# Optimization experiments

Measured on AMD Instinct MI355X. Metric: run time of the kernel, lower is better.

The kernel has to match this reference:

```python
import jax, jax.numpy as jnp
import numpy as np

N, E, G = 50000, 800000, 512
HD, ED, GD, HID = 128, 64, 64, 128  # h_dim, e_dim, g_dim, hid_dim


def _mlp2(x, W1, b1, W2, b2, last_act):
    # Linear -> ReLU -> Linear (-> optional last activation)
    y = jax.nn.relu(x @ W1 + b1) @ W2 + b2
    return last_act(y) if last_act is not None else y


def setup_inputs() -> dict:
    key = jax.random.key(0)
    ks = list(jax.random.split(key, 24))
    ki = iter(ks)

    def p(shape):
        return (jax.random.normal(next(ki), shape, jnp.float32) * 0.02)

    inp = {
        "h": jax.random.normal(next(ki), (N, HD), jnp.float32),
        "e_index": jax.random.randint(next(ki), (2, E), 0, N),
        "e": jax.random.normal(next(ki), (E, ED), jnp.float32),
        "g": jax.random.normal(next(ki), (G, GD), jnp.float32),
        "batch": jnp.sort(jax.random.randint(next(ki), (N,), 0, G)),
        # fc_m: [2*HD+ED+GD, HID, HID], last_activation=relu
        "W_m1": p((2 * HD + ED + GD, HID)), "b_m1": jnp.zeros((HID,), jnp.float32),
        "W_m2": p((HID, HID)), "b_m2": jnp.zeros((HID,), jnp.float32),
        # fc_m_att: [HID, 1], sigmoid
        "W_ma": p((HID, 1)), "b_ma": jnp.zeros((1,), jnp.float32),
        # fc_e: [HID, ED, ED]
        "W_e1": p((HID, ED)), "b_e1": jnp.zeros((ED,), jnp.float32),
        "W_e2": p((ED, ED)), "b_e2": jnp.zeros((ED,), jnp.float32),
        # fc_h: [HD+HID+GD, HD, HD]
        "W_h1": p((HD + HID + GD, HD)), "b_h1": jnp.zeros((HD,), jnp.float32),
        "W_h2": p((HD, HD)), "b_h2": jnp.zeros((HD,), jnp.float32),
        # fc_h_att: [HD, 1]
        "W_ha": p((HD, 1)), "b_ha": jnp.zeros((1,), jnp.float32),
        # fc_g: [GD+HD, GD, GD]
        "W_g1": p((GD + HD, GD)), "b_g1": jnp.zeros((GD,), jnp.float32),
        "W_g2": p((GD, GD)), "b_g2": jnp.zeros((GD,), jnp.float32),
    }
    return inp


def reference(h, e_index, e, g, batch,
              W_m1, b_m1, W_m2, b_m2, W_ma, b_ma,
              W_e1, b_e1, W_e2, b_e2,
              W_h1, b_h1, W_h2, b_h2, W_ha, b_ha,
              W_g1, b_g1, W_g2, b_g2):
    src, dst = e_index[0], e_index[1]
    e_batch = batch[dst]

    # edge message: concat gathered endpoints + edge feat + gathered global
    m_cat = jnp.concatenate([h[src], h[dst], e, g[e_batch]], axis=1)  # [E, 2HD+ED+GD]
    m = jax.nn.relu(jax.nn.relu(m_cat @ W_m1 + b_m1) @ W_m2 + b_m2)   # [E, HID]
    m_att = jax.nn.sigmoid(m @ W_ma + b_ma)                            # [E, 1]

    e_update = _mlp2(m, W_e1, b_e1, W_e2, b_e2, None)                  # [E, ED]
    e_out = jax.nn.relu(e + e_update)

    m_aggr = jax.ops.segment_sum(m_att * m, dst, num_segments=h.shape[0])  # [N, HID]

    h_cat = jnp.concatenate([h, m_aggr, g[batch]], axis=1)             # [N, HD+HID+GD]
    h_update = _mlp2(h_cat, W_h1, b_h1, W_h2, b_h2, None)
    h_out = jax.nn.relu(h + h_update)                                  # [N, HD]
    h_att = h_out @ W_ha + b_ha                                        # [N, 1]

    h_aggr = jax.ops.segment_sum(h_att * h_out, batch, num_segments=g.shape[0])  # [G, HD]

    g_cat = jnp.concatenate([g, h_aggr], axis=1)                       # [G, GD+HD]
    g_update = _mlp2(g_cat, W_g1, b_g1, W_g2, b_g2, None)
    g_out = jax.nn.relu(g + g_update)

    return (h_out, e_out, g_out)
```

## Files before the change

### kernel.cpp

```cpp
#include <hip/hip_runtime.h>
#include <hip/hip_bf16.h>

#define NN 50000
#define NE 800000
#define NG 512
#define HD 128
#define ED 64
#define GD 64
#define HID 128

typedef __attribute__((ext_vector_type(8))) short short8;
typedef __attribute__((ext_vector_type(4))) float f32x4;

__device__ __forceinline__ short f2bf(float f) {
  union { float f; unsigned u; } v; v.f = f;
  unsigned r = v.u + 0x7fffu + ((v.u >> 16) & 1u);
  return (short)(r >> 16);
}

__device__ __forceinline__ float bf2f(short s) {
  union { unsigned u; float f; } v;
  v.u = ((unsigned)(unsigned short)s) << 16;
  return v.f;
}

__device__ __forceinline__ short8 load_a8(const float* p) {
  const f32x4* q = (const f32x4*)p;
  f32x4 x0 = q[0], x1 = q[1];
  short8 r;
  r[0]=f2bf(x0[0]); r[1]=f2bf(x0[1]); r[2]=f2bf(x0[2]); r[3]=f2bf(x0[3]);
  r[4]=f2bf(x1[0]); r[5]=f2bf(x1[1]); r[6]=f2bf(x1[2]); r[7]=f2bf(x1[3]);
  return r;
}

__device__ __forceinline__ int swz(int row, int col, int rowBytes) {
  int b = row * rowBytes + col * 2;
  b ^= (row & 7) << 4;
  return b >> 1;
}

__global__ void pack_kernel(const float* __restrict__ Wm1, const float* __restrict__ Wm2,
                            const float* __restrict__ We1, const float* __restrict__ We2,
                            const float* __restrict__ Wh1, const float* __restrict__ Wh2,
                            short* __restrict__ out) {
  int gid = blockIdx.x * 256 + threadIdx.x;
  if (gid >= 135168) return;
  const float* W; int Ncol, base, idx;
  if (gid < 49152)       { W = Wm1; Ncol = 128; base = 0;      idx = gid; }
  else if (gid < 65536)  { W = Wm2; Ncol = 128; base = 49152;  idx = gid - 49152; }
  else if (gid < 73728)  { W = We1; Ncol = 64;  base = 65536;  idx = gid - 65536; }
  else if (gid < 77824)  { W = We2; Ncol = 64;  base = 73728;  idx = gid - 73728; }
  else if (gid < 118784) { W = Wh1; Ncol = 128; base = 77824;  idx = gid - 77824; }
  else                   { W = Wh2; Ncol = 128; base = 118784; idx = gid - 118784; }
  int k = idx / Ncol, n = idx % Ncol;
  out[base + (k >> 3) * Ncol * 8 + n * 8 + (k & 7)] = f2bf(W[idx]);
}

__global__ void count_kernel(const int* __restrict__ ei, int* __restrict__ deg) {
  int i = blockIdx.x * 256 + threadIdx.x;
  if (i < NE) atomicAdd(&deg[ei[NE + i]], 1);
}

__global__ __launch_bounds__(1024) void scan_kernel(int* __restrict__ deg) {
  __shared__ int psum[1024];
  const int CH = 49;
  int t = threadIdx.x;
  int lo = t * CH, hi = lo + CH; if (hi > NN) hi = NN; if (lo > NN) lo = NN;
  int s = 0;
  for (int i = lo; i < hi; ++i) s += deg[i];
  psum[t] = s;
  __syncthreads();
  for (int d = 1; d < 1024; d <<= 1) {
    int v = (t >= d) ? psum[t - d] : 0;
    __syncthreads();
    psum[t] += v;
    __syncthreads();
  }
  int run = (t == 0) ? 0 : psum[t - 1];
  for (int i = lo; i < hi; ++i) { int v = deg[i]; deg[i] = run; run += v; }
}

__global__ void scatter_kernel(const int* __restrict__ ei, int* __restrict__ off,
                               int* __restrict__ elist) {
  int i = blockIdx.x * 256 + threadIdx.x;
  if (i < NE) {
    int d = ei[NE + i];
    int p = atomicAdd(&off[d], 1);
    elist[p] = i;
  }
}

__global__ __launch_bounds__(256) void edge_kernel(
    const float* __restrict__ h, const int* __restrict__ ei,
    const float* __restrict__ e, const float* __restrict__ g,
    const int* __restrict__ batch, const int* __restrict__ elist,
    const short* __restrict__ pWm1, const float* __restrict__ bm1,
    const short* __restrict__ pWm2, const float* __restrict__ bm2,
    const float* __restrict__ Wma, const float* __restrict__ bma,
    const short* __restrict__ pWe1, const float* __restrict__ be1,
    const short* __restrict__ pWe2, const float* __restrict__ be2,
    float* __restrict__ e_out, float* __restrict__ m_aggr) {
  __shared__ short lds_m[4][16 * 128];
  __shared__ short lds_t[4][16 * 64];
  __shared__ short lds_w[64 * 132];
  __shared__ int sdst[64];

  const int wave = threadIdx.x >> 6;
  const int lane = threadIdx.x & 63;
  const int row16 = lane & 15;
  const int quad = lane >> 4;
  const int pbase = blockIdx.x * 64 + wave * 16;

  const int eidA = elist[pbase + row16];
  const int srcA = ei[eidA];
  const int dstA = ei[NE + eidA];
  const int gbA = batch[dstA];
  if (quad == 0) sdst[wave * 16 + row16] = dstA;

  const float* seg0 = h + (size_t)srcA * HD;
  const float* seg1 = h + (size_t)dstA * HD;
  const float* seg2 = e + (size_t)eidA * ED;
  const float* seg3 = g + (size_t)gbA * GD;

  f32x4 acc[8];
#pragma unroll
  for (int t = 0; t < 8; ++t) acc[t] = (f32x4)0.0f;
#pragma unroll
  for (int c = 0; c < 12; ++c) {
    const float* src; int off;
    if (c < 4)       { src = seg0; off = c * 32; }
    else if (c < 8)  { src = seg1; off = (c - 4) * 32; }
    else if (c < 10) { src = seg2; off = (c - 8) * 32; }
    else             { src = seg3; off = (c - 10) * 32; }
    short8 a = load_a8(src + off + quad * 8);
    const short* bp = pWm1 + (size_t)(c * 4 + quad) * HID * 8 + row16 * 8;
#pragma unroll
    for (int t = 0; t < 8; ++t) {
      short8 b = *(const short8*)(bp + t * 16 * 8);
      acc[t] = __builtin_amdgcn_mfma_f32_16x16x32_bf16(a, b, acc[t], 0, 0, 0);
    }
  }
#pragma unroll
  for (int t = 0; t < 8; ++t) {
    float b1 = bm1[t * 16 + row16];
#pragma unroll
    for (int r = 0; r < 4; ++r) {
      float y = fmaxf(acc[t][r] + b1, 0.f);
      lds_m[wave][swz(quad * 4 + r, t * 16 + row16, 256)] = f2bf(y);
    }
  }

  f32x4 acc2[8];
#pragma unroll
  for (int t = 0; t < 8; ++t) acc2[t] = (f32x4)0.0f;
#pragma unroll
  for (int c = 0; c < 4; ++c) {
    short8 a = *(const short8*)&lds_m[wave][swz(row16, c * 32 + quad * 8, 256)];
    const short* bp = pWm2 + (size_t)(c * 4 + quad) * HID * 8 + row16 * 8;
#pragma unroll
    for (int t = 0; t < 8; ++t) {
      short8 b = *(const short8*)(bp + t * 16 * 8);
      acc2[t] = __builtin_amdgcn_mfma_f32_16x16x32_bf16(a, b, acc2[t], 0, 0, 0);
    }
  }

  float mval[8][4];
#pragma unroll
  for (int t = 0; t < 8; ++t) {
    float b2 = bm2[t * 16 + row16];
#pragma unroll
    for (int r = 0; r < 4; ++r) {
      float y = fmaxf(acc2[t][r] + b2, 0.f);
      mval[t][r] = y;
      lds_m[wave][swz(quad * 4 + r, t * 16 + row16, 256)] = f2bf(y);
    }
  }

  float part[4] = {0.f, 0.f, 0.f, 0.f};
#pragma unroll
  for (int t = 0; t < 8; ++t) {
    float w = Wma[t * 16 + row16];
#pragma unroll
    for (int r = 0; r < 4; ++r) part[r] += mval[t][r] * w;
  }
#pragma unroll
  for (int s = 1; s < 16; s <<= 1) {
#pragma unroll
    for (int r = 0; r < 4; ++r) part[r] += __shfl_xor(part[r], s, 64);
  }
  float bma0 = bma[0];
  float attv[4];
#pragma unroll
  for (int r = 0; r < 4; ++r) attv[r] = 1.f / (1.f + __expf(-(part[r] + bma0)));

#pragma unroll
  for (int t = 0; t < 8; ++t)
#pragma unroll
    for (int r = 0; r < 4; ++r)
      lds_w[(wave * 16 + quad * 4 + r) * 132 + t * 16 + row16] = f2bf(attv[r] * mval[t][r]);

  __syncthreads();

  if (threadIdx.x < 128) {
    int col = threadIdx.x;
    int cur = sdst[0];
    float sum = 0.f;
    int segs = 0;
#pragma unroll 1
    for (int r = 0; r < 64; ++r) {
      int d = sdst[r];
      float v = bf2f(lds_w[r * 132 + col]);
      if (d != cur) {
        if (segs == 0) atomicAdd(&m_aggr[(size_t)cur * HID + col], sum);
        else m_aggr[(size_t)cur * HID + col] = sum;
        cur = d; sum = v; segs = r;
      } else {
        sum += v;
      }
    }
    atomicAdd(&m_aggr[(size_t)cur * HID + col], sum);
  }

  f32x4 acc3[4];
#pragma unroll
  for (int t = 0; t < 4; ++t) acc3[t] = (f32x4)0.0f;
#pragma unroll
  for (int c = 0; c < 4; ++c) {
    short8 a = *(const short8*)&lds_m[wave][swz(row16, c * 32 + quad * 8, 256)];
    const short* bp = pWe1 + (size_t)(c * 4 + quad) * ED * 8 + row16 * 8;
#pragma unroll
    for (int t = 0; t < 4; ++t) {
      short8 b = *(const short8*)(bp + t * 16 * 8);
      acc3[t] = __builtin_amdgcn_mfma_f32_16x16x32_bf16(a, b, acc3[t], 0, 0, 0);
    }
  }
#pragma unroll
  for (int t = 0; t < 4; ++t) {
    float b1 = be1[t * 16 + row16];
#pragma unroll
    for (int r = 0; r < 4; ++r) {
      float y = fmaxf(acc3[t][r] + b1, 0.f);
      lds_t[wave][swz(quad * 4 + r, t * 16 + row16, 128)] = f2bf(y);
    }
  }

  f32x4 acc4[4];
#pragma unroll
  for (int t = 0; t < 4; ++t) acc4[t] = (f32x4)0.0f;
#pragma unroll
  for (int c = 0; c < 2; ++c) {
    short8 a = *(const short8*)&lds_t[wave][swz(row16, c * 32 + quad * 8, 128)];
    const short* bp = pWe2 + (size_t)(c * 4 + quad) * ED * 8 + row16 * 8;
#pragma unroll
    for (int t = 0; t < 4; ++t) {
      short8 b = *(const short8*)(bp + t * 16 * 8);
      acc4[t] = __builtin_amdgcn_mfma_f32_16x16x32_bf16(a, b, acc4[t], 0, 0, 0);
    }
  }
  int eidS[4];
#pragma unroll
  for (int r = 0; r < 4; ++r) eidS[r] = elist[blockIdx.x * 64 + wave * 16 + quad * 4 + r];
#pragma unroll
  for (int t = 0; t < 4; ++t) {
    float b2 = be2[t * 16 + row16];
#pragma unroll
    for (int r = 0; r < 4; ++r) {
      int col = t * 16 + row16;
      float v = e[(size_t)eidS[r] * ED + col] + acc4[t][r] + b2;
      e_out[(size_t)eidS[r] * ED + col] = fmaxf(v, 0.f);
    }
  }
}

__global__ __launch_bounds__(256) void node_kernel(
    const float* __restrict__ h, const float* __restrict__ m_aggr,
    const float* __restrict__ g, const int* __restrict__ batch,
    const short* __restrict__ pWh1, const float* __restrict__ bh1,
    const short* __restrict__ pWh2, const float* __restrict__ bh2,
    const float* __restrict__ Wha, const float* __restrict__ bha,
    float* __restrict__ h_out, float* __restrict__ h_aggr) {
  __shared__ short lds_y[4][16 * 128];
  __shared__ short lds_w2[64 * 132];
  __shared__ int sbat[64];

  const int wave = threadIdx.x >> 6;
  const int lane = threadIdx.x & 63;
  const int row16 = lane & 15;
  const int quad = lane >> 4;
  const int nbase = blockIdx.x * 64 + wave * 16;

  int nA = nbase + row16;
  int nAc = nA < NN ? nA : NN - 1;
  int gbA = batch[nAc];
  if (quad == 0) sbat[wave * 16 + row16] = (nA < NN) ? gbA : -1;
  const float* seg0 = h + (size_t)nAc * HD;
  const float* seg1 = m_aggr + (size_t)nAc * HID;
  const float* seg2 = g + (size_t)gbA * GD;

  f32x4 acc[8];
#pragma unroll
  for (int t = 0; t < 8; ++t) acc[t] = (f32x4)0.0f;
#pragma unroll
  for (int c = 0; c < 10; ++c) {
    const float* src; int off;
    if (c < 4)      { src = seg0; off = c * 32; }
    else if (c < 8) { src = seg1; off = (c - 4) * 32; }
    else            { src = seg2; off = (c - 8) * 32; }
    short8 a = load_a8(src + off + quad * 8);
    const short* bp = pWh1 + (size_t)(c * 4 + quad) * HD * 8 + row16 * 8;
#pragma unroll
    for (int t = 0; t < 8; ++t) {
      short8 b = *(const short8*)(bp + t * 16 * 8);
      acc[t] = __builtin_amdgcn_mfma_f32_16x16x32_bf16(a, b, acc[t], 0, 0, 0);
    }
  }
#pragma unroll
  for (int t = 0; t < 8; ++t) {
    float b1 = bh1[t * 16 + row16];
#pragma unroll
    for (int r = 0; r < 4; ++r) {
      float y = fmaxf(acc[t][r] + b1, 0.f);
      lds_y[wave][swz(quad * 4 + r, t * 16 + row16, 256)] = f2bf(y);
    }
  }

  f32x4 acc2[8];
#pragma unroll
  for (int t = 0; t < 8; ++t) acc2[t] = (f32x4)0.0f;
#pragma unroll
  for (int c = 0; c < 4; ++c) {
    short8 a = *(const short8*)&lds_y[wave][swz(row16, c * 32 + quad * 8, 256)];
    const short* bp = pWh2 + (size_t)(c * 4 + quad) * HD * 8 + row16 * 8;
#pragma unroll
    for (int t = 0; t < 8; ++t) {
      short8 b = *(const short8*)(bp + t * 16 * 8);
      acc2[t] = __builtin_amdgcn_mfma_f32_16x16x32_bf16(a, b, acc2[t], 0, 0, 0);
    }
  }

  float hval[8][4];
  int nS[4];
#pragma unroll
  for (int r = 0; r < 4; ++r) nS[r] = nbase + quad * 4 + r;
#pragma unroll
  for (int t = 0; t < 8; ++t) {
    float b2 = bh2[t * 16 + row16];
#pragma unroll
    for (int r = 0; r < 4; ++r) {
      float v = 0.f;
      if (nS[r] < NN) {
        v = h[(size_t)nS[r] * HD + t * 16 + row16] + acc2[t][r] + b2;
        v = fmaxf(v, 0.f);
        h_out[(size_t)nS[r] * HD + t * 16 + row16] = v;
      }
      hval[t][r] = v;
    }
  }

  float part[4] = {0.f, 0.f, 0.f, 0.f};
#pragma unroll
  for (int t = 0; t < 8; ++t) {
    float w = Wha[t * 16 + row16];
#pragma unroll
    for (int r = 0; r < 4; ++r) part[r] += hval[t][r] * w;
  }
#pragma unroll
  for (int s = 1; s < 16; s <<= 1) {
#pragma unroll
    for (int r = 0; r < 4; ++r) part[r] += __shfl_xor(part[r], s, 64);
  }
  float bha0 = bha[0];
#pragma unroll
  for (int t = 0; t < 8; ++t)
#pragma unroll
    for (int r = 0; r < 4; ++r)
      lds_w2[(wave * 16 + quad * 4 + r) * 132 + t * 16 + row16] =
          f2bf((part[r] + bha0) * hval[t][r]);

  __syncthreads();

  if (threadIdx.x < 128) {
    int col = threadIdx.x;
    int cur = sbat[0];
    float sum = 0.f;
    int segs = 0;
#pragma unroll 1
    for (int r = 0; r < 64; ++r) {
      int d = sbat[r];
      float v = bf2f(lds_w2[r * 132 + col]);
      if (d != cur) {
        if (cur >= 0) {
          if (segs == 0) atomicAdd(&h_aggr[(size_t)cur * HD + col], sum);
          else h_aggr[(size_t)cur * HD + col] = sum;
        }
        cur = d; sum = v; segs = r;
      } else {
        sum += v;
      }
    }
    if (cur >= 0) atomicAdd(&h_aggr[(size_t)cur * HD + col], sum);
  }
}

__global__ void g_kernel(const float* __restrict__ g, const float* __restrict__ h_aggr,
                         const float* __restrict__ Wg1, const float* __restrict__ bg1,
                         const float* __restrict__ Wg2, const float* __restrict__ bg2,
                         float* __restrict__ g_out) {
  __shared__ float cat[192];
  __shared__ float y1[64];
  int r = blockIdx.x;
  int t = threadIdx.x;
  cat[t] = g[(size_t)r * GD + t];
  cat[64 + t] = h_aggr[(size_t)r * HD + t];
  cat[128 + t] = h_aggr[(size_t)r * HD + 64 + t];
  __syncthreads();
  float a = bg1[t];
  for (int k = 0; k < 192; ++k) a += cat[k] * Wg1[k * 64 + t];
  y1[t] = fmaxf(a, 0.f);
  __syncthreads();
  float b = bg2[t];
  for (int k = 0; k < 64; ++k) b += y1[k] * Wg2[k * 64 + t];
  float v = g[(size_t)r * GD + t] + b;
  g_out[(size_t)r * GD + t] = fmaxf(v, 0.f);
}

extern "C" void kernel_launch(void* const* d_in, const int* in_sizes, int n_in,
                              void* d_out, int out_size, void* d_ws, size_t ws_size,
                              hipStream_t stream) {
  const float* h = (const float*)d_in[0];
  const int* ei = (const int*)d_in[1];
  const float* e = (const float*)d_in[2];
  const float* g = (const float*)d_in[3];
  const int* batch = (const int*)d_in[4];
  const float* Wm1 = (const float*)d_in[5];
  const float* bm1 = (const float*)d_in[6];
  const float* Wm2 = (const float*)d_in[7];
  const float* bm2 = (const float*)d_in[8];
  const float* Wma = (const float*)d_in[9];
  const float* bma = (const float*)d_in[10];
  const float* We1 = (const float*)d_in[11];
  const float* be1 = (const float*)d_in[12];
  const float* We2 = (const float*)d_in[13];
  const float* be2 = (const float*)d_in[14];
  const float* Wh1 = (const float*)d_in[15];
  const float* bh1 = (const float*)d_in[16];
  const float* Wh2 = (const float*)d_in[17];
  const float* bh2 = (const float*)d_in[18];
  const float* Wha = (const float*)d_in[19];
  const float* bha = (const float*)d_in[20];
  const float* Wg1 = (const float*)d_in[21];
  const float* bg1 = (const float*)d_in[22];
  const float* Wg2 = (const float*)d_in[23];
  const float* bg2 = (const float*)d_in[24];

  float* out = (float*)d_out;
  float* h_out = out;
  float* e_out = out + (size_t)NN * HD;
  float* g_out = e_out + (size_t)NE * ED;

  char* ws = (char*)d_ws;
  float* m_aggr = (float*)ws;
  float* h_aggr = (float*)(ws + 25600000);
  short* packed = (short*)(ws + 25862144);
  int* deg      = (int*)(ws + 26132480);
  int* elist    = (int*)(ws + 26332480);
  short* pWm1 = packed;
  short* pWm2 = packed + 49152;
  short* pWe1 = packed + 65536;
  short* pWe2 = packed + 73728;
  short* pWh1 = packed + 77824;
  short* pWh2 = packed + 118784;

  hipMemsetAsync(m_aggr, 0, (size_t)NN * HID * 4, stream);
  hipMemsetAsync(h_aggr, 0, (size_t)NG * HD * 4, stream);
  hipMemsetAsync(deg, 0, (size_t)NN * 4, stream);

  pack_kernel<<<(135168 + 255) / 256, 256, 0, stream>>>(Wm1, Wm2, We1, We2, Wh1, Wh2, packed);
  count_kernel<<<(NE + 255) / 256, 256, 0, stream>>>(ei, deg);
  scan_kernel<<<1, 1024, 0, stream>>>(deg);
  scatter_kernel<<<(NE + 255) / 256, 256, 0, stream>>>(ei, deg, elist);

  edge_kernel<<<NE / 64, 256, 0, stream>>>(h, ei, e, g, batch, elist,
                                           pWm1, bm1, pWm2, bm2, Wma, bma,
                                           pWe1, be1, pWe2, be2, e_out, m_aggr);

  node_kernel<<<(NN + 63) / 64, 256, 0, stream>>>(h, m_aggr, g, batch,
                                                  pWh1, bh1, pWh2, bh2, Wha, bha,
                                                  h_out, h_aggr);

  g_kernel<<<NG, 64, 0, stream>>>(g, h_aggr, Wg1, bg1, Wg2, bg2, g_out);
}
```

Measured before the change: 692.0 us.

## Pre-cast node/global features to bf16, hoist gathers, and split segment reduction across all threads

```diff
diff --git a/kernel.cpp b/kernel.cpp
--- a/kernel.cpp
+++ b/kernel.cpp
@@ -10,6 +10,7 @@
 #define HID 128
 
 typedef __attribute__((ext_vector_type(8))) short short8;
+typedef __attribute__((ext_vector_type(4))) short short4v;
 typedef __attribute__((ext_vector_type(4))) float f32x4;
 
 __device__ __forceinline__ short f2bf(float f) {
@@ -56,6 +57,23 @@
   out[base + (k >> 3) * Ncol * 8 + n * 8 + (k & 7)] = f2bf(W[idx]);
 }
 
+__global__ void cast_kernel(const float* __restrict__ h, const float* __restrict__ g,
+                            short* __restrict__ h_bf, short* __restrict__ g_bf) {
+  int gid = blockIdx.x * 256 + threadIdx.x;
+  const int H4 = NN * HD / 4;
+  const int G4 = NG * GD / 4;
+  if (gid < H4) {
+    f32x4 v = ((const f32x4*)h)[gid];
+    short4v r; r[0]=f2bf(v[0]); r[1]=f2bf(v[1]); r[2]=f2bf(v[2]); r[3]=f2bf(v[3]);
+    *(short4v*)(h_bf + gid * 4) = r;
+  } else if (gid < H4 + G4) {
+    int i = gid - H4;
+    f32x4 v = ((const f32x4*)g)[i];
+    short4v r; r[0]=f2bf(v[0]); r[1]=f2bf(v[1]); r[2]=f2bf(v[2]); r[3]=f2bf(v[3]);
+    *(short4v*)(g_bf + i * 4) = r;
+  }
+}
+
 __global__ void count_kernel(const int* __restrict__ ei, int* __restrict__ deg) {
   int i = blockIdx.x * 256 + threadIdx.x;
   if (i < NE) atomicAdd(&deg[ei[NE + i]], 1);
@@ -91,8 +109,8 @@
 }
 
 __global__ __launch_bounds__(256) void edge_kernel(
-    const float* __restrict__ h, const int* __restrict__ ei,
-    const float* __restrict__ e, const float* __restrict__ g,
+    const short* __restrict__ h_bf, const int* __restrict__ ei,
+    const float* __restrict__ e, const short* __restrict__ g_bf,
     const int* __restrict__ batch, const int* __restrict__ elist,
     const short* __restrict__ pWm1, const float* __restrict__ bm1,
     const short* __restrict__ pWm2, const float* __restrict__ bm2,
@@ -102,7 +120,6 @@
     float* __restrict__ e_out, float* __restrict__ m_aggr) {
   __shared__ short lds_m[4][16 * 128];
   __shared__ short lds_t[4][16 * 64];
-  __shared__ short lds_w[64 * 132];
   __shared__ int sdst[64];
 
   const int wave = threadIdx.x >> 6;
@@ -117,27 +134,43 @@
   const int gbA = batch[dstA];
   if (quad == 0) sdst[wave * 16 + row16] = dstA;
 
-  const float* seg0 = h + (size_t)srcA * HD;
-  const float* seg1 = h + (size_t)dstA * HD;
-  const float* seg2 = e + (size_t)eidA * ED;
-  const float* seg3 = g + (size_t)gbA * GD;
+  int eidS[4];
+#pragma unroll
+  for (int r = 0; r < 4; ++r) eidS[r] = elist[pbase + quad * 4 + r];
+
+  short8 afr[12];
+  {
+    const short* s0 = h_bf + (size_t)srcA * HD;
+    const short* s1 = h_bf + (size_t)dstA * HD;
+    const float* s2 = e + (size_t)eidA * ED;
+    const short* s3 = g_bf + (size_t)gbA * GD;
+#pragma unroll
+    for (int c = 0; c < 4; ++c) afr[c] = *(const short8*)(s0 + c * 32 + quad * 8);
+#pragma unroll
+    for (int c = 0; c < 4; ++c) afr[4 + c] = *(const short8*)(s1 + c * 32 + quad * 8);
+    afr[8] = load_a8(s2 + quad * 8);
+    afr[9] = load_a8(s2 + 32 + quad * 8);
+    afr[10] = *(const short8*)(s3 + quad * 8);
+    afr[11] = *(const short8*)(s3 + 32 + quad * 8);
+  }
+
+  float eres[4][4];
+#pragma unroll
+  for (int t = 0; t < 4; ++t)
+#pragma unroll
+    for (int r = 0; r < 4; ++r)
+      eres[t][r] = e[(size_t)eidS[r] * ED + t * 16 + row16];
 
   f32x4 acc[8];
 #pragma unroll
   for (int t = 0; t < 8; ++t) acc[t] = (f32x4)0.0f;
 #pragma unroll
   for (int c = 0; c < 12; ++c) {
-    const float* src; int off;
-    if (c < 4)       { src = seg0; off = c * 32; }
-    else if (c < 8)  { src = seg1; off = (c - 4) * 32; }
-    else if (c < 10) { src = seg2; off = (c - 8) * 32; }
-    else             { src = seg3; off = (c - 10) * 32; }
-    short8 a = load_a8(src + off + quad * 8);
     const short* bp = pWm1 + (size_t)(c * 4 + quad) * HID * 8 + row16 * 8;
 #pragma unroll
     for (int t = 0; t < 8; ++t) {
       short8 b = *(const short8*)(bp + t * 16 * 8);
-      acc[t] = __builtin_amdgcn_mfma_f32_16x16x32_bf16(a, b, acc[t], 0, 0, 0);
+      acc[t] = __builtin_amdgcn_mfma_f32_16x16x32_bf16(afr[c], b, acc[t], 0, 0, 0);
     }
   }
 #pragma unroll
@@ -193,94 +226,92 @@
 #pragma unroll
   for (int r = 0; r < 4; ++r) attv[r] = 1.f / (1.f + __expf(-(part[r] + bma0)));
 
+  f32x4 acc3[4];
+#pragma unroll
+  for (int t = 0; t < 4; ++t) acc3[t] = (f32x4)0.0f;
+#pragma unroll
+  for (int c = 0; c < 4; ++c) {
+    short8 a = *(const short8*)&lds_m[wave][swz(row16, c * 32 + quad * 8, 256)];
+    const short* bp = pWe1 + (size_t)(c * 4 + quad) * ED * 8 + row16 * 8;
+#pragma unroll
+    for (int t = 0; t < 4; ++t) {
+      short8 b = *(const short8*)(bp + t * 16 * 8);
+      acc3[t] = __builtin_amdgcn_mfma_f32_16x16x32_bf16(a, b, acc3[t], 0, 0, 0);
+    }
+  }
+#pragma unroll
+  for (int t = 0; t < 4; ++t) {
+    float b1 = be1[t * 16 + row16];
+#pragma unroll
+    for (int r = 0; r < 4; ++r) {
+      float y = fmaxf(acc3[t][r] + b1, 0.f);
+      lds_t[wave][swz(quad * 4 + r, t * 16 + row16, 128)] = f2bf(y);
+    }
+  }
+
 #pragma unroll
   for (int t = 0; t < 8; ++t)
 #pragma unroll
     for (int r = 0; r < 4; ++r)
-      lds_w[(wave * 16 + quad * 4 + r) * 132 + t * 16 + row16] = f2bf(attv[r] * mval[t][r]);
+      lds_m[wave][swz(quad * 4 + r, t * 16 + row16, 256)] = f2bf(attv[r] * mval[t][r]);
+
+  f32x4 acc4[4];
+#pragma unroll
+  for (int t = 0; t < 4; ++t) acc4[t] = (f32x4)0.0f;
+#pragma unroll
+  for (int c = 0; c < 2; ++c) {
+    short8 a = *(const short8*)&lds_t[wave][swz(row16, c * 32 + quad * 8, 128)];
+    const short* bp = pWe2 + (size_t)(c * 4 + quad) * ED * 8 + row16 * 8;
+#pragma unroll
+    for (int t = 0; t < 4; ++t) {
+      short8 b = *(const short8*)(bp + t * 16 * 8);
+      acc4[t] = __builtin_amdgcn_mfma_f32_16x16x32_bf16(a, b, acc4[t], 0, 0, 0);
+    }
+  }
+#pragma unroll
+  for (int t = 0; t < 4; ++t) {
+    float b2 = be2[t * 16 + row16];
+#pragma unroll
+    for (int r = 0; r < 4; ++r) {
+      int col = t * 16 + row16;
+      float v = eres[t][r] + acc4[t][r] + b2;
+      e_out[(size_t)eidS[r] * ED + col] = fmaxf(v, 0.f);
+    }
+  }
 
   __syncthreads();
 
-  if (threadIdx.x < 128) {
-    int col = threadIdx.x;
-    int cur = sdst[0];
+  {
+    int col = threadIdx.x & 127;
+    int r0 = (threadIdx.x >> 7) * 32;
+    int cur = sdst[r0];
     float sum = 0.f;
-    int segs = 0;
+    bool first = true;
 #pragma unroll 1
-    for (int r = 0; r < 64; ++r) {
+    for (int r = r0; r < r0 + 32; ++r) {
       int d = sdst[r];
-      float v = bf2f(lds_w[r * 132 + col]);
+      float v = bf2f(lds_m[r >> 4][swz(r & 15, col, 256)]);
       if (d != cur) {
-        if (segs == 0) atomicAdd(&m_aggr[(size_t)cur * HID + col], sum);
+        if (first) atomicAdd(&m_aggr[(size_t)cur * HID + col], sum);
         else m_aggr[(size_t)cur * HID + col] = sum;
-        cur = d; sum = v; segs = r;
+        first = false; cur = d; sum = v;
       } else {
         sum += v;
       }
     }
     atomicAdd(&m_aggr[(size_t)cur * HID + col], sum);
   }
-
-  f32x4 acc3[4];
-#pragma unroll
-  for (int t = 0; t < 4; ++t) acc3[t] = (f32x4)0.0f;
-#pragma unroll
-  for (int c = 0; c < 4; ++c) {
-    short8 a = *(const short8*)&lds_m[wave][swz(row16, c * 32 + quad * 8, 256)];
-    const short* bp = pWe1 + (size_t)(c * 4 + quad) * ED * 8 + row16 * 8;
-#pragma unroll
-    for (int t = 0; t < 4; ++t) {
-      short8 b = *(const short8*)(bp + t * 16 * 8);
-      acc3[t] = __builtin_amdgcn_mfma_f32_16x16x32_bf16(a, b, acc3[t], 0, 0, 0);
-    }
-  }
-#pragma unroll
-  for (int t = 0; t < 4; ++t) {
-    float b1 = be1[t * 16 + row16];
-#pragma unroll
-    for (int r = 0; r < 4; ++r) {
-      float y = fmaxf(acc3[t][r] + b1, 0.f);
-      lds_t[wave][swz(quad * 4 + r, t * 16 + row16, 128)] = f2bf(y);
-    }
-  }
-
-  f32x4 acc4[4];
-#pragma unroll
-  for (int t = 0; t < 4; ++t) acc4[t] = (f32x4)0.0f;
-#pragma unroll
-  for (int c = 0; c < 2; ++c) {
-    short8 a = *(const short8*)&lds_t[wave][swz(row16, c * 32 + quad * 8, 128)];
-    const short* bp = pWe2 + (size_t)(c * 4 + quad) * ED * 8 + row16 * 8;
-#pragma unroll
-    for (int t = 0; t < 4; ++t) {
-      short8 b = *(const short8*)(bp + t * 16 * 8);
-      acc4[t] = __builtin_amdgcn_mfma_f32_16x16x32_bf16(a, b, acc4[t], 0, 0, 0);
-    }
-  }
-  int eidS[4];
-#pragma unroll
-  for (int r = 0; r < 4; ++r) eidS[r] = elist[blockIdx.x * 64 + wave * 16 + quad * 4 + r];
-#pragma unroll
-  for (int t = 0; t < 4; ++t) {
-    float b2 = be2[t * 16 + row16];
-#pragma unroll
-    for (int r = 0; r < 4; ++r) {
-      int col = t * 16 + row16;
-      float v = e[(size_t)eidS[r] * ED + col] + acc4[t][r] + b2;
-      e_out[(size_t)eidS[r] * ED + col] = fmaxf(v, 0.f);
-    }
-  }
 }
 
 __global__ __launch_bounds__(256) void node_kernel(
-    const float* __restrict__ h, const float* __restrict__ m_aggr,
-    const float* __restrict__ g, const int* __restrict__ batch,
+    const float* __restrict__ h, const short* __restrict__ h_bf,
+    const float* __restrict__ m_aggr, const short* __restrict__ g_bf,
+    const int* __restrict__ batch,
     const short* __restrict__ pWh1, const float* __restrict__ bh1,
     const short* __restrict__ pWh2, const float* __restrict__ bh2,
     const float* __restrict__ Wha, const float* __restrict__ bha,
     float* __restrict__ h_out, float* __restrict__ h_aggr) {
   __shared__ short lds_y[4][16 * 128];
-  __shared__ short lds_w2[64 * 132];
   __shared__ int sbat[64];
 
   const int wave = threadIdx.x >> 6;
@@ -293,25 +324,30 @@
   int nAc = nA < NN ? nA : NN - 1;
   int gbA = batch[nAc];
   if (quad == 0) sbat[wave * 16 + row16] = (nA < NN) ? gbA : -1;
-  const float* seg0 = h + (size_t)nAc * HD;
-  const float* seg1 = m_aggr + (size_t)nAc * HID;
-  const float* seg2 = g + (size_t)gbA * GD;
+
+  short8 afr[10];
+  {
+    const short* s0 = h_bf + (size_t)nAc * HD;
+    const float* s1 = m_aggr + (size_t)nAc * HID;
+    const short* s2 = g_bf + (size_t)gbA * GD;
+#pragma unroll
+    for (int c = 0; c < 4; ++c) afr[c] = *(const short8*)(s0 + c * 32 + quad * 8);
+#pragma unroll
+    for (int c = 0; c < 4; ++c) afr[4 + c] = load_a8(s1 + c * 32 + quad * 8);
+    afr[8] = *(const short8*)(s2 + quad * 8);
+    afr[9] = *(const short8*)(s2 + 32 + quad * 8);
+  }
 
   f32x4 acc[8];
 #pragma unroll
   for (int t = 0; t < 8; ++t) acc[t] = (f32x4)0.0f;
 #pragma unroll
   for (int c = 0; c < 10; ++c) {
-    const float* src; int off;
-    if (c < 4)      { src = seg0; off = c * 32; }
-    else if (c < 8) { src = seg1; off = (c - 4) * 32; }
-    else            { src = seg2; off = (c - 8) * 32; }
-    short8 a = load_a8(src + off + quad * 8);
     const short* bp = pWh1 + (size_t)(c * 4 + quad) * HD * 8 + row16 * 8;
 #pragma unroll
     for (int t = 0; t < 8; ++t) {
       short8 b = *(const short8*)(bp + t * 16 * 8);
-      acc[t] = __builtin_amdgcn_mfma_f32_16x16x32_bf16(a, b, acc[t], 0, 0, 0);
+      acc[t] = __builtin_amdgcn_mfma_f32_16x16x32_bf16(afr[c], b, acc[t], 0, 0, 0);
     }
   }
 #pragma unroll
@@ -374,26 +410,27 @@
   for (int t = 0; t < 8; ++t)
 #pragma unroll
     for (int r = 0; r < 4; ++r)
-      lds_w2[(wave * 16 + quad * 4 + r) * 132 + t * 16 + row16] =
+      lds_y[wave][swz(quad * 4 + r, t * 16 + row16, 256)] =
           f2bf((part[r] + bha0) * hval[t][r]);
 
   __syncthreads();
 
-  if (threadIdx.x < 128) {
-    int col = threadIdx.x;
-    int cur = sbat[0];
+  {
+    int col = threadIdx.x & 127;
+    int r0 = (threadIdx.x >> 7) * 32;
+    int cur = sbat[r0];
     float sum = 0.f;
-    int segs = 0;
+    bool first = true;
 #pragma unroll 1
-    for (int r = 0; r < 64; ++r) {
+    for (int r = r0; r < r0 + 32; ++r) {
       int d = sbat[r];
-      float v = bf2f(lds_w2[r * 132 + col]);
+      float v = bf2f(lds_y[r >> 4][swz(r & 15, col, 256)]);
       if (d != cur) {
         if (cur >= 0) {
-          if (segs == 0) atomicAdd(&h_aggr[(size_t)cur * HD + col], sum);
+          if (first) atomicAdd(&h_aggr[(size_t)cur * HD + col], sum);
           else h_aggr[(size_t)cur * HD + col] = sum;
         }
-        cur = d; sum = v; segs = r;
+        first = false; cur = d; sum = v;
       } else {
         sum += v;
       }
@@ -464,6 +501,8 @@
   short* packed = (short*)(ws + 25862144);
   int* deg      = (int*)(ws + 26132480);
   int* elist    = (int*)(ws + 26332480);
+  short* h_bf   = (short*)(ws + 29532480);
+  short* g_bf   = (short*)(ws + 42332480);
   short* pWm1 = packed;
   short* pWm2 = packed + 49152;
   short* pWe1 = packed + 65536;
@@ -476,15 +515,16 @@
   hipMemsetAsync(deg, 0, (size_t)NN * 4, stream);
 
   pack_kernel<<<(135168 + 255) / 256, 256, 0, stream>>>(Wm1, Wm2, We1, We2, Wh1, Wh2, packed);
+  cast_kernel<<<(1608192 + 255) / 256, 256, 0, stream>>>(h, g, h_bf, g_bf);
   count_kernel<<<(NE + 255) / 256, 256, 0, stream>>>(ei, deg);
   scan_kernel<<<1, 1024, 0, stream>>>(deg);
   scatter_kernel<<<(NE + 255) / 256, 256, 0, stream>>>(ei, deg, elist);
 
-  edge_kernel<<<NE / 64, 256, 0, stream>>>(h, ei, e, g, batch, elist,
+  edge_kernel<<<NE / 64, 256, 0, stream>>>(h_bf, ei, e, g_bf, batch, elist,
                                            pWm1, bm1, pWm2, bm2, Wma, bma,
                                            pWe1, be1, pWe2, be2, e_out, m_aggr);
 
-  node_kernel<<<(NN + 63) / 64, 256, 0, stream>>>(h, m_aggr, g, batch,
+  node_kernel<<<(NN + 63) / 64, 256, 0, stream>>>(h, h_bf, m_aggr, g_bf, batch,
                                                   pWh1, bh1, pWh2, bh2, Wha, bha,
                                                   h_out, h_aggr);
 
```

Result: slower. 728.7 us (+5.3%).
